# Kernel tuning notes

Hardware: AMD Instinct MI355X
Metric: run time of the kernel (lower is better)

The kernel has to match this reference:

```python
import jax, jax.numpy as jnp
import numpy as np
import math

B, S, D, H, M, R = 4, 1024, 1024, 16, 4, 64
DH = D // H
EPS = 1e-8

def setup_inputs() -> dict:
    key = jax.random.key(0)
    ks = jax.random.split(key, 8)
    sc = 0.02
    return {
        'x': jax.random.normal(ks[0], (B, S, D), jnp.float32),
        'Wk': jax.random.normal(ks[1], (D, D), jnp.float32) * sc,
        'bk': jnp.zeros((D,), jnp.float32),
        'Wq': jax.random.normal(ks[2], (D, D), jnp.float32) * sc,
        'bq': jnp.zeros((D,), jnp.float32),
        'Wv': jax.random.normal(ks[3], (D, D), jnp.float32) * sc,
        'bv': jnp.zeros((D,), jnp.float32),
        'mask1': jax.random.normal(ks[4], (M, R, S), jnp.float32) * sc,
        'mask2': jax.random.normal(ks[5], (M, R, S), jnp.float32) * sc,
        'roll_back': jax.random.randint(ks[6], (M, S, S), 0, S, jnp.int64),
    }

def reference(x, Wk, bk, Wq, bq, Wv, bv, mask1, mask2, roll_back):
    def proj(W, b):
        # torch Linear: x @ W^T + b ; reshape to [B, H, S, DH]
        y = jnp.dot(x, W.T) + b
        return y.reshape(B, S, H, DH).transpose(0, 2, 1, 3)
    k = proj(Wk, bk)
    q = proj(Wq, bq)
    v = proj(Wv, bv)
    # learnable low-rank mask: [M, S, S]
    learnable_mask = jnp.einsum('mrs,mrt->mst', mask1, mask2)
    # gather along last dim with roll_back indices
    gathered = jnp.take_along_axis(learnable_mask, roll_back, axis=-1)  # [M, S, S]
    att = jnp.einsum('bhsd,bhtd->bhst', q, k) / math.sqrt(DH)  # [B, H, S, S]
    att = att.reshape(B, H // M, M, S, S) * gathered[None, None]
    att = att.reshape(B, H, S, S)
    # Frobenius norm over last two dims per (B, H)
    fro = jnp.sqrt(jnp.sum(att * att, axis=(-2, -1), keepdims=True))
    att = att / (fro + EPS)
    out = jnp.einsum('bhst,bhtd->bhsd', att, v)
    return out.transpose(0, 2, 1, 3).reshape(B, S, D)
```

## Files before the change

kernel.cpp:

```cpp
#include <hip/hip_runtime.h>
#include <hip/hip_bf16.h>
#include <stdint.h>

typedef __attribute__((ext_vector_type(8))) __bf16 bf16x8;
typedef __attribute__((ext_vector_type(4))) float  f32x4;

__device__ __forceinline__ ushort f2bf(float f) {
    union { float f; uint32_t u; } v; v.f = f;
    uint32_t u = v.u;
    uint32_t r = 0x7FFFu + ((u >> 16) & 1u);
    return (ushort)((u + r) >> 16);
}
__device__ __forceinline__ float bf2f(ushort u) {
    union { uint32_t u; float f; } v; v.u = ((uint32_t)u) << 16;
    return v.f;
}

typedef __attribute__((address_space(3))) uint32_t lds_u32_t;
typedef const __attribute__((address_space(1))) uint32_t glb_u32_t;
__device__ __forceinline__ void async_copy16(const void* g, void* l) {
    __builtin_amdgcn_global_load_lds((glb_u32_t*)g, (lds_u32_t*)l, 16, 0, 0);
}

__global__ __launch_bounds__(256) void convert_all(
    const float* __restrict__ x, const float* __restrict__ wk,
    const float* __restrict__ wq, const float* __restrict__ wv,
    ushort* __restrict__ xb, ushort* __restrict__ wball)
{
    int i = blockIdx.x * 256 + threadIdx.x;
    const float* src; ushort* dst; int j;
    if (i < 1048576) { src = x; dst = xb; j = i; }
    else {
        int t = i - 1048576;
        int z = t >> 18;
        j = t & 262143;
        src = (z == 0) ? wk : (z == 1) ? wq : wv;
        dst = wball + z * 1048576;
    }
    float4 f = ((const float4*)src)[j];
    ushort4 o;
    o.x = f2bf(f.x); o.y = f2bf(f.y); o.z = f2bf(f.z); o.w = f2bf(f.w);
    ((ushort4*)dst)[j] = o;
}

__global__ __launch_bounds__(256, 2) void proj_gemm(
    const ushort* __restrict__ xb, const ushort* __restrict__ wball,
    const float* __restrict__ bk, const float* __restrict__ bq, const float* __restrict__ bv,
    ushort* __restrict__ kd, ushort* __restrict__ qd, ushort* __restrict__ vd)
{
    __shared__ ushort As[2][128 * 64];
    __shared__ ushort Bs[2][128 * 64];
    const int z = blockIdx.z;
    const int row0 = blockIdx.x * 128;
    const int col0 = blockIdx.y * 128;
    const ushort* wb = wball + z * 1048576;
    const int tid = threadIdx.x;
    const int lane = tid & 63, wave = tid >> 6;
    const int quad = lane >> 4, m15 = lane & 15;
    const int wr = wave >> 1, wc = wave & 1;

    f32x4 acc[4][4];
    for (int i = 0; i < 4; i++)
        for (int j = 0; j < 4; j++) acc[i][j] = (f32x4){0.f, 0.f, 0.f, 0.f};

    auto stage = [&](int buf, int kk) {
        #pragma unroll
        for (int i = 0; i < 4; i++) {
            int c = tid + i * 256;
            int r = c >> 3, cjp = c & 7;
            int cj = cjp ^ (r & 7);
            async_copy16(&xb[(row0 + r) * 1024 + kk + cj * 8], &As[buf][c * 8]);
            async_copy16(&wb[(col0 + r) * 1024 + kk + cj * 8], &Bs[buf][c * 8]);
        }
    };

    stage(0, 0);
    for (int it = 0; it < 16; it++) {
        __syncthreads();
        if (it < 15) stage((it + 1) & 1, (it + 1) * 64);
        const ushort* Ab = As[it & 1];
        const ushort* Bb = Bs[it & 1];
        #pragma unroll
        for (int kh = 0; kh < 2; kh++) {
            bf16x8 af[4], bfv[4];
            #pragma unroll
            for (int fr = 0; fr < 4; fr++) {
                int row = wr * 64 + fr * 16 + m15;
                int q4 = kh * 4 + quad;
                af[fr] = *(const bf16x8*)&Ab[row * 64 + ((q4 ^ (row & 7)) * 8)];
            }
            #pragma unroll
            for (int fc = 0; fc < 4; fc++) {
                int row = wc * 64 + fc * 16 + m15;
                int q4 = kh * 4 + quad;
                bfv[fc] = *(const bf16x8*)&Bb[row * 64 + ((q4 ^ (row & 7)) * 8)];
            }
            #pragma unroll
            for (int fr = 0; fr < 4; fr++)
                #pragma unroll
                for (int fc = 0; fc < 4; fc++)
                    acc[fr][fc] = __builtin_amdgcn_mfma_f32_16x16x32_bf16(af[fr], bfv[fc], acc[fr][fc], 0, 0, 0);
        }
    }

    const float* bias = (z == 0) ? bk : (z == 1) ? bq : bv;
    ushort* dstA = (z == 0) ? kd : qd;
    for (int fr = 0; fr < 4; fr++) {
        int ibase = row0 + wr * 64 + fr * 16 + quad * 4;
        int b_ = ibase >> 10, s = ibase & 1023;
        for (int fc = 0; fc < 4; fc++) {
            int j = col0 + wc * 64 + fc * 16 + m15;
            int h = j >> 6, dh = j & 63;
            float bb = bias[j];
            if (z < 2) {
                for (int r = 0; r < 4; r++)
                    dstA[((b_ * 16 + h) * 1024 + (s + r)) * 64 + dh] = f2bf(acc[fr][fc][r] + bb);
            } else {
                ushort4 o;
                o.x = f2bf(acc[fr][fc][0] + bb);
                o.y = f2bf(acc[fr][fc][1] + bb);
                o.z = f2bf(acc[fr][fc][2] + bb);
                o.w = f2bf(acc[fr][fc][3] + bb);
                *(ushort4*)&vd[((b_ * 16 + h) * 64 + dh) * 1024 + s] = o;
            }
        }
    }
}

__global__ __launch_bounds__(256) void mask_fused(
    const float* __restrict__ m1, const float* __restrict__ m2,
    const int* __restrict__ rb, ushort* __restrict__ gth)
{
    __shared__ float As8[64 * 8];
    __shared__ float lmS[8 * 1024];
    const int s0 = blockIdx.x * 8;
    const int m = blockIdx.y;
    const int tid = threadIdx.x;

    if (tid < 128) {
        int r = tid >> 1, half = tid & 1;
        *(float4*)&As8[r * 8 + half * 4] =
            *(const float4*)&m1[(m * 64 + r) * 1024 + s0 + half * 4];
    }
    __syncthreads();

    f32x4 acc8[8];
    #pragma unroll
    for (int s = 0; s < 8; s++) acc8[s] = (f32x4){0.f, 0.f, 0.f, 0.f};
    const float* m2b = m2 + m * 65536 + tid * 4;
    #pragma unroll 4
    for (int r = 0; r < 64; r++) {
        float4 b4 = *(const float4*)&m2b[r * 1024];
        f32x4 b = (f32x4){b4.x, b4.y, b4.z, b4.w};
        #pragma unroll
        for (int s = 0; s < 8; s++) {
            float a = As8[r * 8 + s];
            acc8[s] += a * b;
        }
    }
    #pragma unroll
    for (int s = 0; s < 8; s++)
        *(f32x4*)&lmS[s * 1024 + tid * 4] = acc8[s];
    __syncthreads();

    const int base = (m * 1024 + s0) * 1024;
    #pragma unroll
    for (int i = 0; i < 8; i++) {
        int c = tid + i * 256;
        int row = c >> 8, j = (c & 255) * 4;
        int4 idx = *(const int4*)&rb[base + row * 1024 + j];
        ushort4 o;
        o.x = f2bf(lmS[row * 1024 + (idx.x & 1023)] * 0.125f);
        o.y = f2bf(lmS[row * 1024 + (idx.y & 1023)] * 0.125f);
        o.z = f2bf(lmS[row * 1024 + (idx.z & 1023)] * 0.125f);
        o.w = f2bf(lmS[row * 1024 + (idx.w & 1023)] * 0.125f);
        *(ushort4*)&gth[base + row * 1024 + j] = o;
    }
}

__global__ __launch_bounds__(256, 2) void attention(
    const ushort* __restrict__ qd, const ushort* __restrict__ kd, const ushort* __restrict__ vd,
    const ushort* __restrict__ gth, float* __restrict__ O, float* __restrict__ ss)
{
    __shared__ ushort Ks[2][64 * 64];
    __shared__ ushort Vs[2][64 * 64];
    __shared__ ushort Ms[2][64 * 64];
    __shared__ ushort Ps[64 * 72];
    __shared__ float red[4];
    const int s0 = blockIdx.x * 64;
    const int bh = blockIdx.y;
    const int mm = bh & 3;
    const int tid = threadIdx.x, lane = tid & 63, wave = tid >> 6;
    const int quad = lane >> 4, m15 = lane & 15;
    const ushort* gbase = gth + mm * 1048576 + s0 * 1024;

    #pragma unroll
    for (int i = 0; i < 2; i++) {
        int c = tid + i * 256;
        int r = c >> 3, cj = (c & 7) ^ (r & 7);
        async_copy16(&qd[(bh * 1024 + s0 + r) * 64 + cj * 8], &Ks[0][c * 8]);
    }
    __syncthreads();
    bf16x8 qf[2];
    {
        int row = wave * 16 + m15;
        #pragma unroll
        for (int kk = 0; kk < 2; kk++)
            qf[kk] = *(const bf16x8*)&Ks[0][row * 64 + (((kk * 4 + quad) ^ (row & 7)) * 8)];
    }
    __syncthreads();

    f32x4 oacc[4];
    #pragma unroll
    for (int i = 0; i < 4; i++) oacc[i] = (f32x4){0.f, 0.f, 0.f, 0.f};
    float ssacc = 0.f;

    auto stage = [&](int buf, int t0) {
        #pragma unroll
        for (int i = 0; i < 2; i++) {
            int c = tid + i * 256;
            int r = c >> 3, cj = (c & 7) ^ (r & 7);
            async_copy16(&kd[(bh * 1024 + t0 + r) * 64 + cj * 8], &Ks[buf][c * 8]);
            async_copy16(&vd[(bh * 64 + r) * 1024 + t0 + cj * 8], &Vs[buf][c * 8]);
            async_copy16(&gbase[r * 1024 + t0 + cj * 8],          &Ms[buf][c * 8]);
        }
    };

    stage(0, 0);
    for (int it = 0; it < 16; it++) {
        __syncthreads();
        if (it < 15) stage((it + 1) & 1, (it + 1) * 64);
        const ushort* Kb = Ks[it & 1];
        const ushort* Vb = Vs[it & 1];
        const ushort* Mb = Ms[it & 1];

        f32x4 pacc[4];
        #pragma unroll
        for (int tc = 0; tc < 4; tc++) {
            f32x4 p = (f32x4){0.f, 0.f, 0.f, 0.f};
            #pragma unroll
            for (int kk = 0; kk < 2; kk++) {
                int row = tc * 16 + m15;
                bf16x8 b = *(const bf16x8*)&Kb[row * 64 + (((kk * 4 + quad) ^ (row & 7)) * 8)];
                p = __builtin_amdgcn_mfma_f32_16x16x32_bf16(qf[kk], b, p, 0, 0, 0);
            }
            pacc[tc] = p;
        }
        #pragma unroll
        for (int tc = 0; tc < 4; tc++) {
            int col = tc * 16 + m15;
            #pragma unroll
            for (int r = 0; r < 4; r++) {
                int sr = wave * 16 + quad * 4 + r;
                float mv = bf2f(Mb[sr * 64 + (((col >> 3) ^ (sr & 7)) * 8) + (col & 7)]);
                float pv = pacc[tc][r] * mv;
                ssacc += pv * pv;
                Ps[sr * 72 + col] = f2bf(pv);
            }
        }
        bf16x8 af[2];
        #pragma unroll
        for (int kk = 0; kk < 2; kk++)
            af[kk] = *(const bf16x8*)&Ps[(wave * 16 + m15) * 72 + kk * 32 + quad * 8];
        #pragma unroll
        for (int nc = 0; nc < 4; nc++) {
            #pragma unroll
            for (int kk = 0; kk < 2; kk++) {
                int row = nc * 16 + m15;
                bf16x8 b = *(const bf16x8*)&Vb[row * 64 + (((kk * 4 + quad) ^ (row & 7)) * 8)];
                oacc[nc] = __builtin_amdgcn_mfma_f32_16x16x32_bf16(af[kk], b, oacc[nc], 0, 0, 0);
            }
        }
    }
    #pragma unroll
    for (int nc = 0; nc < 4; nc++)
        #pragma unroll
        for (int r = 0; r < 4; r++) {
            int s = s0 + wave * 16 + quad * 4 + r;
            O[(bh * 1024 + s) * 64 + nc * 16 + m15] = oacc[nc][r];
        }
    for (int off = 32; off; off >>= 1) ssacc += __shfl_down(ssacc, off, 64);
    if (lane == 0) red[wave] = ssacc;
    __syncthreads();
    if (tid == 0) atomicAdd(&ss[bh], red[0] + red[1] + red[2] + red[3]);
}

__global__ __launch_bounds__(256) void normalize_out(const float* __restrict__ O,
                                                     const float* __restrict__ ss,
                                                     float* __restrict__ out)
{
    int gid = blockIdx.x * 256 + threadIdx.x;
    int e = gid * 4;
    int bh = e >> 16;
    float inv = 1.f / (sqrtf(ss[bh]) + 1e-8f);
    float4 v4 = *(const float4*)&O[e];
    int b_ = bh >> 4, h = bh & 15;
    int s = (e >> 6) & 1023, dh = e & 63;
    float4 o4 = {v4.x * inv, v4.y * inv, v4.z * inv, v4.w * inv};
    *(float4*)&out[((b_ * 1024 + s) * 16 + h) * 64 + dh] = o4;
}

extern "C" void kernel_launch(void* const* d_in, const int* in_sizes, int n_in,
                              void* d_out, int out_size, void* d_ws, size_t ws_size,
                              hipStream_t stream) {
    const float* x  = (const float*)d_in[0];
    const float* Wk = (const float*)d_in[1];
    const float* bk = (const float*)d_in[2];
    const float* Wq = (const float*)d_in[3];
    const float* bq = (const float*)d_in[4];
    const float* Wv = (const float*)d_in[5];
    const float* bv = (const float*)d_in[6];
    const float* m1 = (const float*)d_in[7];
    const float* m2 = (const float*)d_in[8];
    const int*   rb = (const int*)d_in[9];
    float* out = (float*)d_out;

    char* ws = (char*)d_ws;
    ushort* xb    = (ushort*)(ws);
    ushort* wball = (ushort*)(ws + 8388608);
    ushort* kd    = (ushort*)(ws + 14680064);
    ushort* qd    = (ushort*)(ws + 23068672);
    ushort* vd    = (ushort*)(ws + 31457280);
    float*  O     = (float*)(ws + 39845888);
    ushort* gth   = (ushort*)(ws + 56623104);
    float*  ssb   = (float*)(ws + 65011712);

    convert_all<<<7168, 256, 0, stream>>>(x, Wk, Wq, Wv, xb, wball);
    proj_gemm<<<dim3(32, 8, 3), 256, 0, stream>>>(xb, wball, bk, bq, bv, kd, qd, vd);
    mask_fused<<<dim3(128, 4), 256, 0, stream>>>(m1, m2, rb, gth);
    hipMemsetAsync(ssb, 0, 64 * sizeof(float), stream);
    attention<<<dim3(16, 64), 256, 0, stream>>>(qd, kd, vd, gth, O, ssb);
    normalize_out<<<4096, 256, 0, stream>>>(O, ssb, out);
}
```

Measured before the change: 213.1 us.

## Fuse mask build into convert kernel, remap grids, transpose attention MFMA operands

The fp32-to-bf16 conversion and the low-rank mask gather now run in one launch, so one kernel boundary goes away. Proj_gemm and attention switch to 1D grids with remapped block indices, aiming at better L2 locality. Attention swaps the MFMA operand order so each lane holds the output transposed. This allows vectorized mask reads and packed P writes to LDS, and O is staged through LDS for coalesced float4 global stores. The cost is extra LDS for the O staging buffer, which may lower occupancy, plus the added complexity of several combined changes.

```diff
diff --git a/kernel.cpp b/kernel.cpp
--- a/kernel.cpp
+++ b/kernel.cpp
@@ -15,6 +15,9 @@
     union { uint32_t u; float f; } v; v.u = ((uint32_t)u) << 16;
     return v.f;
 }
+__device__ __forceinline__ uint32_t pack2bf(float a, float b) {
+    return (uint32_t)f2bf(a) | ((uint32_t)f2bf(b) << 16);
+}
 
 typedef __attribute__((address_space(3))) uint32_t lds_u32_t;
 typedef const __attribute__((address_space(1))) uint32_t glb_u32_t;
@@ -22,25 +25,69 @@
     __builtin_amdgcn_global_load_lds((glb_u32_t*)g, (lds_u32_t*)l, 16, 0, 0);
 }
 
-__global__ __launch_bounds__(256) void convert_all(
+__global__ __launch_bounds__(256) void prep(
     const float* __restrict__ x, const float* __restrict__ wk,
     const float* __restrict__ wq, const float* __restrict__ wv,
-    ushort* __restrict__ xb, ushort* __restrict__ wball)
+    const float* __restrict__ m1, const float* __restrict__ m2,
+    const int* __restrict__ rb,
+    ushort* __restrict__ xb, ushort* __restrict__ wball, ushort* __restrict__ gth)
 {
-    int i = blockIdx.x * 256 + threadIdx.x;
-    const float* src; ushort* dst; int j;
-    if (i < 1048576) { src = x; dst = xb; j = i; }
-    else {
-        int t = i - 1048576;
-        int z = t >> 18;
-        j = t & 262143;
-        src = (z == 0) ? wk : (z == 1) ? wq : wv;
-        dst = wball + z * 1048576;
-    }
-    float4 f = ((const float4*)src)[j];
-    ushort4 o;
-    o.x = f2bf(f.x); o.y = f2bf(f.y); o.z = f2bf(f.z); o.w = f2bf(f.w);
-    ((ushort4*)dst)[j] = o;
+    __shared__ float As8[64 * 8];
+    __shared__ float lmS[8 * 1024];
+    const int tid = threadIdx.x;
+    if (blockIdx.x >= 512) {
+        int i = (blockIdx.x - 512) * 256 + tid;
+        const float* src; ushort* dst; int j;
+        if (i < 1048576) { src = x; dst = xb; j = i; }
+        else {
+            int t = i - 1048576;
+            int z = t >> 18;
+            j = t & 262143;
+            src = (z == 0) ? wk : (z == 1) ? wq : wv;
+            dst = wball + z * 1048576;
+        }
+        float4 f = ((const float4*)src)[j];
+        ushort4 o;
+        o.x = f2bf(f.x); o.y = f2bf(f.y); o.z = f2bf(f.z); o.w = f2bf(f.w);
+        ((ushort4*)dst)[j] = o;
+        return;
+    }
+    const int s0 = (blockIdx.x & 127) * 8;
+    const int m = blockIdx.x >> 7;
+    if (tid < 128) {
+        int r = tid >> 1, half = tid & 1;
+        *(float4*)&As8[r * 8 + half * 4] =
+            *(const float4*)&m1[(m * 64 + r) * 1024 + s0 + half * 4];
+    }
+    __syncthreads();
+    f32x4 acc8[8];
+    #pragma unroll
+    for (int s = 0; s < 8; s++) acc8[s] = (f32x4){0.f, 0.f, 0.f, 0.f};
+    const float* m2b = m2 + m * 65536 + tid * 4;
+    #pragma unroll 4
+    for (int r = 0; r < 64; r++) {
+        float4 b4 = *(const float4*)&m2b[r * 1024];
+        f32x4 b = (f32x4){b4.x, b4.y, b4.z, b4.w};
+        #pragma unroll
+        for (int s = 0; s < 8; s++) acc8[s] += As8[r * 8 + s] * b;
+    }
+    #pragma unroll
+    for (int s = 0; s < 8; s++)
+        *(f32x4*)&lmS[s * 1024 + tid * 4] = acc8[s];
+    __syncthreads();
+    const int base = (m * 1024 + s0) * 1024;
+    #pragma unroll
+    for (int i = 0; i < 8; i++) {
+        int c = tid + i * 256;
+        int row = c >> 8, j = (c & 255) * 4;
+        int4 idx = *(const int4*)&rb[base + row * 1024 + j];
+        ushort4 o;
+        o.x = f2bf(lmS[row * 1024 + (idx.x & 1023)] * 0.125f);
+        o.y = f2bf(lmS[row * 1024 + (idx.y & 1023)] * 0.125f);
+        o.z = f2bf(lmS[row * 1024 + (idx.z & 1023)] * 0.125f);
+        o.w = f2bf(lmS[row * 1024 + (idx.w & 1023)] * 0.125f);
+        *(ushort4*)&gth[base + row * 1024 + j] = o;
+    }
 }
 
 __global__ __launch_bounds__(256, 2) void proj_gemm(
@@ -50,9 +97,11 @@
 {
     __shared__ ushort As[2][128 * 64];
     __shared__ ushort Bs[2][128 * 64];
-    const int z = blockIdx.z;
-    const int row0 = blockIdx.x * 128;
-    const int col0 = blockIdx.y * 128;
+    const int g = blockIdx.x;
+    const int col0 = (g & 7) * 128;
+    const int t = g >> 3;
+    const int row0 = (t & 31) * 128;
+    const int z = t >> 5;
     const ushort* wb = wball + z * 1048576;
     const int tid = threadIdx.x;
     const int lane = tid & 63, wave = tid >> 6;
@@ -93,7 +142,7 @@
             for (int fc = 0; fc < 4; fc++) {
                 int row = wc * 64 + fc * 16 + m15;
                 int q4 = kh * 4 + quad;
-                bfv[fc] = *(const bf16x8*)&Bb[row * 64 + ((q4 ^ (row & 7)) * 8)];
+                bfv[fc] = *(const bf16x8*)&Bs[it & 1][row * 64 + ((q4 ^ (row & 7)) * 8)];
             }
             #pragma unroll
             for (int fr = 0; fr < 4; fr++)
@@ -127,57 +176,6 @@
     }
 }
 
-__global__ __launch_bounds__(256) void mask_fused(
-    const float* __restrict__ m1, const float* __restrict__ m2,
-    const int* __restrict__ rb, ushort* __restrict__ gth)
-{
-    __shared__ float As8[64 * 8];
-    __shared__ float lmS[8 * 1024];
-    const int s0 = blockIdx.x * 8;
-    const int m = blockIdx.y;
-    const int tid = threadIdx.x;
-
-    if (tid < 128) {
-        int r = tid >> 1, half = tid & 1;
-        *(float4*)&As8[r * 8 + half * 4] =
-            *(const float4*)&m1[(m * 64 + r) * 1024 + s0 + half * 4];
-    }
-    __syncthreads();
-
-    f32x4 acc8[8];
-    #pragma unroll
-    for (int s = 0; s < 8; s++) acc8[s] = (f32x4){0.f, 0.f, 0.f, 0.f};
-    const float* m2b = m2 + m * 65536 + tid * 4;
-    #pragma unroll 4
-    for (int r = 0; r < 64; r++) {
-        float4 b4 = *(const float4*)&m2b[r * 1024];
-        f32x4 b = (f32x4){b4.x, b4.y, b4.z, b4.w};
-        #pragma unroll
-        for (int s = 0; s < 8; s++) {
-            float a = As8[r * 8 + s];
-            acc8[s] += a * b;
-        }
-    }
-    #pragma unroll
-    for (int s = 0; s < 8; s++)
-        *(f32x4*)&lmS[s * 1024 + tid * 4] = acc8[s];
-    __syncthreads();
-
-    const int base = (m * 1024 + s0) * 1024;
-    #pragma unroll
-    for (int i = 0; i < 8; i++) {
-        int c = tid + i * 256;
-        int row = c >> 8, j = (c & 255) * 4;
-        int4 idx = *(const int4*)&rb[base + row * 1024 + j];
-        ushort4 o;
-        o.x = f2bf(lmS[row * 1024 + (idx.x & 1023)] * 0.125f);
-        o.y = f2bf(lmS[row * 1024 + (idx.y & 1023)] * 0.125f);
-        o.z = f2bf(lmS[row * 1024 + (idx.z & 1023)] * 0.125f);
-        o.w = f2bf(lmS[row * 1024 + (idx.w & 1023)] * 0.125f);
-        *(ushort4*)&gth[base + row * 1024 + j] = o;
-    }
-}
-
 __global__ __launch_bounds__(256, 2) void attention(
     const ushort* __restrict__ qd, const ushort* __restrict__ kd, const ushort* __restrict__ vd,
     const ushort* __restrict__ gth, float* __restrict__ O, float* __restrict__ ss)
@@ -186,12 +184,17 @@
     __shared__ ushort Vs[2][64 * 64];
     __shared__ ushort Ms[2][64 * 64];
     __shared__ ushort Ps[64 * 72];
+    __shared__ float Osc[64 * 68];
     __shared__ float red[4];
-    const int s0 = blockIdx.x * 64;
-    const int bh = blockIdx.y;
+    const int g = blockIdx.x;
+    const int idx = g >> 3;
+    const int s0 = (idx & 15) * 64;
+    const int bh = (g & 7) + 8 * (idx >> 4);
     const int mm = bh & 3;
     const int tid = threadIdx.x, lane = tid & 63, wave = tid >> 6;
     const int quad = lane >> 4, m15 = lane & 15;
+    const int sw = wave * 16 + m15;
+    const int sw7 = m15 & 7;
     const ushort* gbase = gth + mm * 1048576 + s0 * 1024;
 
     #pragma unroll
@@ -202,12 +205,9 @@
     }
     __syncthreads();
     bf16x8 qf[2];
-    {
-        int row = wave * 16 + m15;
-        #pragma unroll
-        for (int kk = 0; kk < 2; kk++)
-            qf[kk] = *(const bf16x8*)&Ks[0][row * 64 + (((kk * 4 + quad) ^ (row & 7)) * 8)];
-    }
+    #pragma unroll
+    for (int kk = 0; kk < 2; kk++)
+        qf[kk] = *(const bf16x8*)&Ks[0][sw * 64 + (((kk * 4 + quad) ^ sw7) * 8)];
     __syncthreads();
 
     f32x4 oacc[4];
@@ -241,44 +241,51 @@
             #pragma unroll
             for (int kk = 0; kk < 2; kk++) {
                 int row = tc * 16 + m15;
-                bf16x8 b = *(const bf16x8*)&Kb[row * 64 + (((kk * 4 + quad) ^ (row & 7)) * 8)];
-                p = __builtin_amdgcn_mfma_f32_16x16x32_bf16(qf[kk], b, p, 0, 0, 0);
+                bf16x8 a = *(const bf16x8*)&Kb[row * 64 + (((kk * 4 + quad) ^ (row & 7)) * 8)];
+                p = __builtin_amdgcn_mfma_f32_16x16x32_bf16(a, qf[kk], p, 0, 0, 0);
             }
             pacc[tc] = p;
         }
         #pragma unroll
         for (int tc = 0; tc < 4; tc++) {
-            int col = tc * 16 + m15;
-            #pragma unroll
-            for (int r = 0; r < 4; r++) {
-                int sr = wave * 16 + quad * 4 + r;
-                float mv = bf2f(Mb[sr * 64 + (((col >> 3) ^ (sr & 7)) * 8) + (col & 7)]);
-                float pv = pacc[tc][r] * mv;
-                ssacc += pv * pv;
-                Ps[sr * 72 + col] = f2bf(pv);
-            }
-        }
-        bf16x8 af[2];
+            int ch = (tc * 2 + (quad >> 1)) ^ sw7;
+            ushort4 mv4 = *(const ushort4*)&Mb[sw * 64 + ch * 8 + (quad & 1) * 4];
+            float p0 = pacc[tc][0] * bf2f(mv4.x);
+            float p1 = pacc[tc][1] * bf2f(mv4.y);
+            float p2 = pacc[tc][2] * bf2f(mv4.z);
+            float p3 = pacc[tc][3] * bf2f(mv4.w);
+            ssacc += p0 * p0 + p1 * p1 + p2 * p2 + p3 * p3;
+            uint2 pw;
+            pw.x = pack2bf(p0, p1);
+            pw.y = pack2bf(p2, p3);
+            *(uint2*)&Ps[sw * 72 + tc * 16 + quad * 4] = pw;
+        }
+        bf16x8 pf[2];
         #pragma unroll
         for (int kk = 0; kk < 2; kk++)
-            af[kk] = *(const bf16x8*)&Ps[(wave * 16 + m15) * 72 + kk * 32 + quad * 8];
+            pf[kk] = *(const bf16x8*)&Ps[sw * 72 + kk * 32 + quad * 8];
         #pragma unroll
         for (int nc = 0; nc < 4; nc++) {
             #pragma unroll
             for (int kk = 0; kk < 2; kk++) {
                 int row = nc * 16 + m15;
-                bf16x8 b = *(const bf16x8*)&Vb[row * 64 + (((kk * 4 + quad) ^ (row & 7)) * 8)];
-                oacc[nc] = __builtin_amdgcn_mfma_f32_16x16x32_bf16(af[kk], b, oacc[nc], 0, 0, 0);
-            }
-        }
-    }
+                bf16x8 a = *(const bf16x8*)&Vb[row * 64 + (((kk * 4 + quad) ^ (row & 7)) * 8)];
+                oacc[nc] = __builtin_amdgcn_mfma_f32_16x16x32_bf16(a, pf[kk], oacc[nc], 0, 0, 0);
+            }
+        }
+    }
+    __syncthreads();
     #pragma unroll
     for (int nc = 0; nc < 4; nc++)
-        #pragma unroll
-        for (int r = 0; r < 4; r++) {
-            int s = s0 + wave * 16 + quad * 4 + r;
-            O[(bh * 1024 + s) * 64 + nc * 16 + m15] = oacc[nc][r];
-        }
+        *(f32x4*)&Osc[sw * 68 + nc * 16 + quad * 4] = oacc[nc];
+    __syncthreads();
+    #pragma unroll
+    for (int i = 0; i < 4; i++) {
+        int c = tid + i * 256;
+        int row = c >> 4, col = (c & 15) * 4;
+        f32x4 v4 = *(const f32x4*)&Osc[row * 68 + col];
+        *(f32x4*)&O[(bh * 1024 + s0 + row) * 64 + col] = v4;
+    }
     for (int off = 32; off; off >>= 1) ssacc += __shfl_down(ssacc, off, 64);
     if (lane == 0) red[wave] = ssacc;
     __syncthreads();
@@ -325,10 +332,9 @@
     ushort* gth   = (ushort*)(ws + 56623104);
     float*  ssb   = (float*)(ws + 65011712);
 
-    convert_all<<<7168, 256, 0, stream>>>(x, Wk, Wq, Wv, xb, wball);
-    proj_gemm<<<dim3(32, 8, 3), 256, 0, stream>>>(xb, wball, bk, bq, bv, kd, qd, vd);
-    mask_fused<<<dim3(128, 4), 256, 0, stream>>>(m1, m2, rb, gth);
+    prep<<<7680, 256, 0, stream>>>(x, Wk, Wq, Wv, m1, m2, rb, xb, wball, gth);
+    proj_gemm<<<768, 256, 0, stream>>>(xb, wball, bk, bq, bv, kd, qd, vd);
     hipMemsetAsync(ssb, 0, 64 * sizeof(float), stream);
-    attention<<<dim3(16, 64), 256, 0, stream>>>(qd, kd, vd, gth, O, ssb);
+    attention<<<1024, 256, 0, stream>>>(qd, kd, vd, gth, O, ssb);
     normalize_out<<<4096, 256, 0, stream>>>(O, ssb, out);
 }
```

New measurement: 206.8 us. -3.0%, faster.
